# Kernel optimization log

Measured on AMD Instinct MI355X. Metric: run time of the kernel, lower is better.

The kernel has to match this reference:

```python
import jax, jax.numpy as jnp
from jax import lax
import numpy as np

B, D, H, W = 1, 20, 96, 96
N = B * (D - 4) * H * W  # one 7x7x7 guide patch per output voxel
DN = ('NCDHW', 'OIDHW', 'NCDHW')


def _conv3(x, w, b):
    # Conv3d(1,1,kernel=3,stride=1,VALID) + bias
    y = lax.conv_general_dilated(x, w, (1, 1, 1), 'VALID', dimension_numbers=DN)
    return y + b[None, :, None, None, None]


def _guide_branch(x, w1, b1, w2, b2):
    # nn.Sequential(Conv3d, ReLU, Conv3d, ReLU): 7^3 -> 5^3 -> 3^3
    return jax.nn.relu(_conv3(jax.nn.relu(_conv3(x, w1, b1)), w2, b2))


def setup_inputs() -> dict:
    key = jax.random.key(0)
    ks = jax.random.split(key, 12)
    s = 1.0 / np.sqrt(27.0)  # torch Conv3d default init scale (fan_in = 1*3*3*3)
    return {
        'x': jax.random.normal(ks[0], (B, 1, D, H, W), jnp.float32),
        'domain_neighbor': jax.random.uniform(ks[1], (1, 1, 7, 7, 7), jnp.float32),
        'guide_im': jax.random.normal(ks[2], (N, 1, 7, 7, 7), jnp.float32),
        'w1_d': jax.random.normal(ks[3], (1, 1, 3, 3, 3), jnp.float32) * s,
        'b1_d': jax.random.normal(ks[4], (1,), jnp.float32) * s,
        'w2_d': jax.random.normal(ks[5], (1, 1, 3, 3, 3), jnp.float32) * s,
        'b2_d': jax.random.normal(ks[6], (1,), jnp.float32) * s,
        'w1_r': jax.random.normal(ks[7], (1, 1, 3, 3, 3), jnp.float32) * s,
        'b1_r': jax.random.normal(ks[8], (1,), jnp.float32) * s,
        'w2_r': jax.random.normal(ks[9], (1, 1, 3, 3, 3), jnp.float32) * s,
        'b2_r': jax.random.normal(ks[10], (1,), jnp.float32) * s,
    }


def reference(x, domain_neighbor, guide_im, w1_d, b1_d, w2_d, b2_d,
              w1_r, b1_r, w2_r, b2_r):
    Bx, _, Dx, Hx, Wx = x.shape
    # kernel-generating guide nets
    domain_kernel = _guide_branch(domain_neighbor, w1_d, b1_d, w2_d, b2_d)  # (1,1,3,3,3)
    range_kernel = _guide_branch(guide_im, w1_r, b1_r, w2_r, b2_r)          # (N,1,3,3,3)
    weights = (domain_kernel * range_kernel + 1e-10).reshape(-1, 27)        # (N,27)
    # pad H,W by 1 (depth unpadded), extract all 3x3x3 patches (feature order d,h,w)
    xp = jnp.pad(x, ((0, 0), (0, 0), (0, 0), (1, 1), (1, 1)))
    p = lax.conv_general_dilated_patches(xp, (3, 3, 3), (1, 1, 1), 'VALID',
                                         dimension_numbers=DN)  # (B,27,D-2,H,W)
    p = p[:, :, 1:-1]  # keep the D-4 center-aligned depth windows (matches mat_size)
    p = p.transpose(0, 2, 3, 4, 1).reshape(-1, 27)  # (N,27)
    out = jnp.sum(weights * p, axis=1) / jnp.sum(weights, axis=1)  # weighted local mean
    return out.reshape(Bx, 1, Dx - 4, Hx, Wx)
```

## Files before the change

### kernel.cpp

```cpp
#include <hip/hip_runtime.h>
#include <hip/hip_fp16.h>


#define NPATCH 147456
#define TPB     256
#define PPB      64
#define NBLK   (NPATCH / PPB)
#define ROW_H     8
#define PATCH_H 392
#define PATCH_D 196
#define NROWS  (PPB * 49)
#define NRD      13

typedef float f4u __attribute__((ext_vector_type(4), aligned(4)));
typedef float f2u __attribute__((ext_vector_type(2), aligned(4)));

__global__ __launch_bounds__(128) void domain_branch_kernel(
    const float* __restrict__ dn,
    const float* __restrict__ w1, const float* __restrict__ b1,
    const float* __restrict__ w2, const float* __restrict__ b2,
    float* __restrict__ dom_out)
{
    __shared__ float s_in[344];
    __shared__ float s_c1[128];
    const int t = threadIdx.x;
    for (int idx = t; idx < 343; idx += 128) s_in[idx] = dn[idx];
    __syncthreads();
    if (t < 125) {
        const int i = t / 25, j = (t / 5) % 5, k = t % 5;
        float acc = b1[0];
        const float* base = &s_in[i * 49 + j * 7 + k];
#pragma unroll
        for (int dz = 0; dz < 3; ++dz)
#pragma unroll
            for (int dy = 0; dy < 3; ++dy)
#pragma unroll
                for (int dx = 0; dx < 3; ++dx)
                    acc = fmaf(base[dz * 49 + dy * 7 + dx], w1[dz * 9 + dy * 3 + dx], acc);
        s_c1[t] = fmaxf(acc, 0.f);
    }
    __syncthreads();
    if (t < 27) {
        const int dz = t / 9, dy = (t / 3) % 3, dx = t % 3;
        float acc = b2[0];
#pragma unroll
        for (int u = 0; u < 3; ++u)
#pragma unroll
            for (int v = 0; v < 3; ++v)
#pragma unroll
                for (int q = 0; q < 3; ++q)
                    acc = fmaf(s_c1[(dz + u) * 25 + (dy + v) * 5 + (dx + q)],
                               w2[u * 9 + v * 3 + q], acc);
        dom_out[t] = fmaxf(acc, 0.f);
    }
}

__device__ __forceinline__ float h2f_lo(unsigned int q) {
    return __half2float(__ushort_as_half((unsigned short)(q & 0xffffu)));
}
__device__ __forceinline__ float h2f_hi(unsigned int q) {
    return __half2float(__ushort_as_half((unsigned short)(q >> 16)));
}
__device__ __forceinline__ unsigned int pkh(float lo, float hi) {
    return __builtin_bit_cast(unsigned int, __builtin_amdgcn_cvt_pkrtz(lo, hi));
}

__device__ __forceinline__ void load_row(const unsigned int* __restrict__ P, float* d,
                                         int zi, int y) {
    const int d0 = zi * 28 + y * 4;
    const uint4 q = *reinterpret_cast<const uint4*>(P + d0);
    d[0] = h2f_lo(q.x); d[1] = h2f_hi(q.x);
    d[2] = h2f_lo(q.y); d[3] = h2f_hi(q.y);
    d[4] = h2f_lo(q.z); d[5] = h2f_hi(q.z);
    d[6] = h2f_lo(q.w);
}

template<int IB, int JB, int IE, int JE>
__device__ __forceinline__ void run_tasks(const unsigned int* __restrict__ P,
                                          const float* __restrict__ w1, float bb1,
                                          const float* __restrict__ w2,
                                          float (&a2)[3][3][3])
{
#pragma unroll
    for (int i = IB; i <= IE; ++i) {
        float rw[3][3][7];
        const int j0 = (i == IB) ? JB : 0;
        const int j1 = (i == IE) ? JE : 4;
#pragma unroll
        for (int j = j0; j <= j1; ++j) {
            if (j == j0) {
#pragma unroll
                for (int u = 0; u < 3; ++u)
#pragma unroll
                    for (int dy = 0; dy < 3; ++dy)
                        load_row(P, rw[u][(j + dy) % 3], i + u, j + dy);
            } else {
#pragma unroll
                for (int u = 0; u < 3; ++u)
                    load_row(P, rw[u][(j + 2) % 3], i + u, j + 2);
            }

            float c1r[5];
#pragma unroll
            for (int k = 0; k < 5; ++k) {
                float a = bb1;
#pragma unroll
                for (int u = 0; u < 3; ++u)
#pragma unroll
                    for (int v = 0; v < 3; ++v) {
                        const float* rr = rw[u][(j + v) % 3];
#pragma unroll
                        for (int w = 0; w < 3; ++w)
                            a = fmaf(rr[k + w], w1[u * 9 + v * 3 + w], a);
                    }
                c1r[k] = fmaxf(a, 0.f);
            }

#pragma unroll
            for (int dz2 = 0; dz2 < 3; ++dz2) {
                const int u2 = i - dz2;
                if (u2 >= 0 && u2 < 3) {
#pragma unroll
                    for (int v2 = 0; v2 < 3; ++v2) {
                        const int dy2 = j - v2;
                        if (dy2 >= 0 && dy2 < 3) {
#pragma unroll
                            for (int dx2 = 0; dx2 < 3; ++dx2)
#pragma unroll
                                for (int q = 0; q < 3; ++q)
                                    a2[dz2][dy2][dx2] =
                                        fmaf(c1r[dx2 + q],
                                             w2[u2 * 9 + v2 * 3 + q],
                                             a2[dz2][dy2][dx2]);
                        }
                    }
                }
            }
        }
    }
}

__global__ __launch_bounds__(TPB, 2) void jbf_main_kernel(
    const float* __restrict__ guide, const float* __restrict__ x,
    const float* __restrict__ w1, const float* __restrict__ b1,
    const float* __restrict__ w2, const float* __restrict__ b2,
    const float* __restrict__ dom, float* __restrict__ out)
{
    union SM {
        unsigned short tile[PPB * PATCH_H];
        float part[3][PPB][27];
    };
    __shared__ SM sm;

    const int tid  = threadIdx.x;
    const int wid  = tid >> 6;
    const int lane = tid & 63;
    const int blk  = blockIdx.x;
    const int n    = blk * PPB + lane;

    {
        const float* __restrict__ srcf = guide + (size_t)blk * (PPB * 343);
        unsigned int* __restrict__ tdw = reinterpret_cast<unsigned int*>(sm.tile);

        f4u A[NRD]; f2u B[NRD]; float C[NRD];
#pragma unroll
        for (int rd = 0; rd < NRD; ++rd) {
            int idx = tid + rd * TPB;
            if (idx > NROWS - 1) idx = NROWS - 1;
            const int p = idx / 49, r = idx - p * 49;
            const float* s = srcf + p * 343 + r * 7;
            A[rd] = *reinterpret_cast<const f4u*>(s);
            B[rd] = *reinterpret_cast<const f2u*>(s + 4);
            C[rd] = s[6];
        }
        __builtin_amdgcn_sched_barrier(0);
#pragma unroll
        for (int rd = 0; rd < NRD; ++rd) {
            if (rd < 12 || tid < NROWS - 12 * TPB) {
                const int idx = tid + rd * TPB;
                const int p = idx / 49, r = idx - p * 49;
                uint4 q;
                q.x = pkh(A[rd].x, A[rd].y); q.y = pkh(A[rd].z, A[rd].w);
                q.z = pkh(B[rd].x, B[rd].y); q.w = pkh(C[rd], 0.f);
                *reinterpret_cast<uint4*>(tdw + p * PATCH_D + r * 4) = q;
            }
        }
    }
    __syncthreads();

    const unsigned int* __restrict__ P =
        reinterpret_cast<const unsigned int*>(sm.tile) + lane * PATCH_D;
    const float bb1 = b1[0];

    float a2[3][3][3];
    {
        const float init = (wid == 0) ? b2[0] : 0.f;
#pragma unroll
        for (int a = 0; a < 3; ++a)
#pragma unroll
            for (int b = 0; b < 3; ++b)
#pragma unroll
                for (int c = 0; c < 3; ++c) a2[a][b][c] = init;
    }

    if      (wid == 0) run_tasks<0, 0, 1, 1>(P, w1, bb1, w2, a2);
    else if (wid == 1) run_tasks<1, 2, 2, 3>(P, w1, bb1, w2, a2);
    else if (wid == 2) run_tasks<2, 4, 3, 4>(P, w1, bb1, w2, a2);
    else               run_tasks<4, 0, 4, 4>(P, w1, bb1, w2, a2);

    __syncthreads();

    if (wid != 0) {
#pragma unroll
        for (int t = 0; t < 27; ++t)
            sm.part[wid - 1][lane][t] = a2[t / 9][(t / 3) % 3][t % 3];
    }
    __syncthreads();

    if (wid == 0) {
        const int dd  = n / 9216;
        const int rem = n - dd * 9216;
        const int h   = rem / 96;
        const int w_  = rem - h * 96;

        float num = 0.f, den = 0.f;
#pragma unroll
        for (int dz = 0; dz < 3; ++dz)
#pragma unroll
            for (int dy = 0; dy < 3; ++dy)
#pragma unroll
                for (int dx = 0; dx < 3; ++dx) {
                    const int t = dz * 9 + dy * 3 + dx;
                    const float r2 = fmaxf(a2[dz][dy][dx] + sm.part[0][lane][t]
                                           + sm.part[1][lane][t]
                                           + sm.part[2][lane][t], 0.f);
                    const float wt = fmaf(dom[t], r2, 1e-10f);
                    const int yy = h - 1 + dy, xx = w_ - 1 + dx;
                    float xv = 0.f;
                    if (yy >= 0 && yy < 96 && xx >= 0 && xx < 96)
                        xv = x[(dd + 1 + dz) * 9216 + yy * 96 + xx];
                    num = fmaf(wt, xv, num);
                    den += wt;
                }
        out[n] = num / den;
    }
}

extern "C" void kernel_launch(void* const* d_in, const int* in_sizes, int n_in,
                              void* d_out, int out_size, void* d_ws, size_t ws_size,
                              hipStream_t stream) {
    const float* x     = (const float*)d_in[0];
    const float* dn    = (const float*)d_in[1];
    const float* guide = (const float*)d_in[2];
    const float* w1_d  = (const float*)d_in[3];
    const float* b1_d  = (const float*)d_in[4];
    const float* w2_d  = (const float*)d_in[5];
    const float* b2_d  = (const float*)d_in[6];
    const float* w1_r  = (const float*)d_in[7];
    const float* b1_r  = (const float*)d_in[8];
    const float* w2_r  = (const float*)d_in[9];
    const float* b2_r  = (const float*)d_in[10];
    float* out = (float*)d_out;
    float* dom = (float*)d_ws;

    domain_branch_kernel<<<1, 128, 0, stream>>>(dn, w1_d, b1_d, w2_d, b2_d, dom);
    jbf_main_kernel<<<NBLK, TPB, 0, stream>>>(guide, x, w1_r, b1_r, w2_r,
                                              b2_r, dom, out);
}
```

Baseline: 46.26 us.

## Make main kernel persistent with a producer wave double-buffering guide tiles

The main kernel becomes persistent: 256 blocks each loop over 9 tiles of 64 patches. One wave acts as a producer, loading and fp16-packing the next tile into a second LDS buffer while the other three waves compute on the current tile. Wave 0 also finishes the previous tile's weighted-mean epilogue inside the loop. This aims to hide global-load latency behind compute, but leaves only three compute waves per block and one block per CU (launch_bounds 256,1). It also needs about 116 KB of dynamic LDS, so occupancy drops.

```diff
diff --git a/kernel.cpp b/kernel.cpp
--- a/kernel.cpp
+++ b/kernel.cpp
@@ -2,15 +2,17 @@
 #include <hip/hip_fp16.h>
 
 
-#define NPATCH 147456
-#define TPB     256
+#define NPATCH   147456
+#define TPB      256
 #define PPB      64
-#define NBLK   (NPATCH / PPB)
-#define ROW_H     8
-#define PATCH_H 392
-#define PATCH_D 196
-#define NROWS  (PPB * 49)
-#define NRD      13
+#define NTILES   (NPATCH / PPB)
+#define NBLOCK   256
+#define TPBLK    (NTILES / NBLOCK)
+#define PATCH_H  392
+#define PATCH_D  196
+#define NROWS    (PPB * 49)
+#define BUF_H    (PPB * PATCH_H)
+#define SMEM_BYTES (2 * BUF_H * 2 + 2 * 2 * PPB * 27 * 4)
 
 typedef float f4u __attribute__((ext_vector_type(4), aligned(4)));
 typedef float f2u __attribute__((ext_vector_type(2), aligned(4)));
@@ -140,31 +142,57 @@
     }
 }
 
-__global__ __launch_bounds__(TPB, 2) void jbf_main_kernel(
+template<int CNT>
+__device__ __forceinline__ void stage_chunk(const float* __restrict__ srcf,
+                                            unsigned int* __restrict__ dwbuf,
+                                            int& p, int& rem) {
+    f4u A[CNT]; f2u B[CNT]; float C[CNT];
+    int pl = p, rl = rem;
+#pragma unroll
+    for (int k = 0; k < CNT; ++k) {
+        const float* s = srcf + pl * 343 + rl * 7;
+        A[k] = *reinterpret_cast<const f4u*>(s);
+        B[k] = *reinterpret_cast<const f2u*>(s + 4);
+        C[k] = s[6];
+        pl += 1; rl += 15; if (rl >= 49) { rl -= 49; pl += 1; }
+    }
+    __builtin_amdgcn_sched_barrier(0);
+    pl = p; rl = rem;
+#pragma unroll
+    for (int k = 0; k < CNT; ++k) {
+        uint4 q;
+        q.x = pkh(A[k].x, A[k].y); q.y = pkh(A[k].z, A[k].w);
+        q.z = pkh(B[k].x, B[k].y); q.w = pkh(C[k], 0.f);
+        *reinterpret_cast<uint4*>(dwbuf + pl * PATCH_D + rl * 4) = q;
+        pl += 1; rl += 15; if (rl >= 49) { rl -= 49; pl += 1; }
+    }
+    p = pl; rem = rl;
+}
+
+__global__ __launch_bounds__(TPB, 1) void jbf_main_kernel(
     const float* __restrict__ guide, const float* __restrict__ x,
     const float* __restrict__ w1, const float* __restrict__ b1,
     const float* __restrict__ w2, const float* __restrict__ b2,
     const float* __restrict__ dom, float* __restrict__ out)
 {
-    union SM {
-        unsigned short tile[PPB * PATCH_H];
-        float part[3][PPB][27];
-    };
-    __shared__ SM sm;
-
-    const int tid  = threadIdx.x;
-    const int wid  = tid >> 6;
-    const int lane = tid & 63;
-    const int blk  = blockIdx.x;
-    const int n    = blk * PPB + lane;
+    extern __shared__ unsigned char smem[];
+    unsigned short* buf  = reinterpret_cast<unsigned short*>(smem);
+    float*          part = reinterpret_cast<float*>(smem + 2 * BUF_H * 2);
+
+    const int tid   = threadIdx.x;
+    const int wid   = tid >> 6;
+    const int lane  = tid & 63;
+    const int tile0 = blockIdx.x * TPBLK;
+
+    const float bb1 = b1[0];
+    const float bb2 = b2[0];
 
     {
-        const float* __restrict__ srcf = guide + (size_t)blk * (PPB * 343);
-        unsigned int* __restrict__ tdw = reinterpret_cast<unsigned int*>(sm.tile);
-
-        f4u A[NRD]; f2u B[NRD]; float C[NRD];
-#pragma unroll
-        for (int rd = 0; rd < NRD; ++rd) {
+        const float* __restrict__ srcf = guide + (size_t)tile0 * (PPB * 343);
+        unsigned int* __restrict__ tdw = reinterpret_cast<unsigned int*>(buf);
+        f4u A[13]; f2u B[13]; float C[13];
+#pragma unroll
+        for (int rd = 0; rd < 13; ++rd) {
             int idx = tid + rd * TPB;
             if (idx > NROWS - 1) idx = NROWS - 1;
             const int p = idx / 49, r = idx - p * 49;
@@ -175,7 +203,7 @@
         }
         __builtin_amdgcn_sched_barrier(0);
 #pragma unroll
-        for (int rd = 0; rd < NRD; ++rd) {
+        for (int rd = 0; rd < 13; ++rd) {
             if (rd < 12 || tid < NROWS - 12 * TPB) {
                 const int idx = tid + rd * TPB;
                 const int p = idx / 49, r = idx - p * 49;
@@ -188,41 +216,85 @@
     }
     __syncthreads();
 
-    const unsigned int* __restrict__ P =
-        reinterpret_cast<const unsigned int*>(sm.tile) + lane * PATCH_D;
-    const float bb1 = b1[0];
-
     float a2[3][3][3];
-    {
-        const float init = (wid == 0) ? b2[0] : 0.f;
-#pragma unroll
-        for (int a = 0; a < 3; ++a)
-#pragma unroll
-            for (int b = 0; b < 3; ++b)
-#pragma unroll
-                for (int c = 0; c < 3; ++c) a2[a][b][c] = init;
-    }
-
-    if      (wid == 0) run_tasks<0, 0, 1, 1>(P, w1, bb1, w2, a2);
-    else if (wid == 1) run_tasks<1, 2, 2, 3>(P, w1, bb1, w2, a2);
-    else if (wid == 2) run_tasks<2, 4, 3, 4>(P, w1, bb1, w2, a2);
-    else               run_tasks<4, 0, 4, 4>(P, w1, bb1, w2, a2);
-
-    __syncthreads();
-
-    if (wid != 0) {
-#pragma unroll
-        for (int t = 0; t < 27; ++t)
-            sm.part[wid - 1][lane][t] = a2[t / 9][(t / 3) % 3][t % 3];
-    }
-    __syncthreads();
+
+#pragma unroll 1
+    for (int t = 0; t < TPBLK; ++t) {
+        unsigned int* curd = reinterpret_cast<unsigned int*>(buf + (t & 1) * BUF_H);
+
+        if (wid == 3) {
+            if (t + 1 < TPBLK) {
+                const float* __restrict__ srcf =
+                    guide + (size_t)(tile0 + t + 1) * (PPB * 343);
+                unsigned int* __restrict__ nxtd =
+                    reinterpret_cast<unsigned int*>(buf + ((t + 1) & 1) * BUF_H);
+                int p = lane / 49, rem = lane - (lane / 49) * 49;
+                stage_chunk<17>(srcf, nxtd, p, rem);
+                stage_chunk<16>(srcf, nxtd, p, rem);
+                stage_chunk<16>(srcf, nxtd, p, rem);
+            }
+        } else if (wid == 0) {
+            if (t > 0) {
+                const int n   = (tile0 + t - 1) * PPB + lane;
+                const float* pb = part + ((t - 1) & 1) * (2 * PPB * 27);
+                const int dd  = n / 9216;
+                const int rm  = n - dd * 9216;
+                const int h   = rm / 96;
+                const int w_  = rm - h * 96;
+                float num = 0.f, den = 0.f;
+#pragma unroll
+                for (int dz = 0; dz < 3; ++dz)
+#pragma unroll
+                    for (int dy = 0; dy < 3; ++dy)
+#pragma unroll
+                        for (int dx = 0; dx < 3; ++dx) {
+                            const int tt = dz * 9 + dy * 3 + dx;
+                            const float r2 = fmaxf(a2[dz][dy][dx]
+                                                   + pb[(0 * PPB + lane) * 27 + tt]
+                                                   + pb[(1 * PPB + lane) * 27 + tt], 0.f);
+                            const float wt = fmaf(dom[tt], r2, 1e-10f);
+                            const int yy = h - 1 + dy, xx = w_ - 1 + dx;
+                            float xv = 0.f;
+                            if (yy >= 0 && yy < 96 && xx >= 0 && xx < 96)
+                                xv = x[(dd + 1 + dz) * 9216 + yy * 96 + xx];
+                            num = fmaf(wt, xv, num);
+                            den += wt;
+                        }
+                out[n] = num / den;
+            }
+#pragma unroll
+            for (int a = 0; a < 3; ++a)
+#pragma unroll
+                for (int b = 0; b < 3; ++b)
+#pragma unroll
+                    for (int c = 0; c < 3; ++c) a2[a][b][c] = bb2;
+            run_tasks<0, 0, 1, 3>(curd + lane * PATCH_D, w1, bb1, w2, a2);
+        } else {
+            float al[3][3][3];
+#pragma unroll
+            for (int a = 0; a < 3; ++a)
+#pragma unroll
+                for (int b = 0; b < 3; ++b)
+#pragma unroll
+                    for (int c = 0; c < 3; ++c) al[a][b][c] = 0.f;
+            if (wid == 1) run_tasks<1, 4, 3, 1>(curd + lane * PATCH_D, w1, bb1, w2, al);
+            else          run_tasks<3, 2, 4, 4>(curd + lane * PATCH_D, w1, bb1, w2, al);
+            float* pb = part + (t & 1) * (2 * PPB * 27) + ((wid - 1) * PPB + lane) * 27;
+#pragma unroll
+            for (int tt = 0; tt < 27; ++tt)
+                pb[tt] = al[tt / 9][(tt / 3) % 3][tt % 3];
+        }
+        __syncthreads();
+    }
 
     if (wid == 0) {
+        const int t = TPBLK - 1;
+        const int n   = (tile0 + t) * PPB + lane;
+        const float* pb = part + (t & 1) * (2 * PPB * 27);
         const int dd  = n / 9216;
-        const int rem = n - dd * 9216;
-        const int h   = rem / 96;
-        const int w_  = rem - h * 96;
-
+        const int rm  = n - dd * 9216;
+        const int h   = rm / 96;
+        const int w_  = rm - h * 96;
         float num = 0.f, den = 0.f;
 #pragma unroll
         for (int dz = 0; dz < 3; ++dz)
@@ -230,11 +302,11 @@
             for (int dy = 0; dy < 3; ++dy)
 #pragma unroll
                 for (int dx = 0; dx < 3; ++dx) {
-                    const int t = dz * 9 + dy * 3 + dx;
-                    const float r2 = fmaxf(a2[dz][dy][dx] + sm.part[0][lane][t]
-                                           + sm.part[1][lane][t]
-                                           + sm.part[2][lane][t], 0.f);
-                    const float wt = fmaf(dom[t], r2, 1e-10f);
+                    const int tt = dz * 9 + dy * 3 + dx;
+                    const float r2 = fmaxf(a2[dz][dy][dx]
+                                           + pb[(0 * PPB + lane) * 27 + tt]
+                                           + pb[(1 * PPB + lane) * 27 + tt], 0.f);
+                    const float wt = fmaf(dom[tt], r2, 1e-10f);
                     const int yy = h - 1 + dy, xx = w_ - 1 + dx;
                     float xv = 0.f;
                     if (yy >= 0 && yy < 96 && xx >= 0 && xx < 96)
@@ -263,7 +335,10 @@
     float* out = (float*)d_out;
     float* dom = (float*)d_ws;
 
+    hipFuncSetAttribute((const void*)jbf_main_kernel,
+                        hipFuncAttributeMaxDynamicSharedMemorySize, SMEM_BYTES);
+
     domain_branch_kernel<<<1, 128, 0, stream>>>(dn, w1_d, b1_d, w2_d, b2_d, dom);
-    jbf_main_kernel<<<NBLK, TPB, 0, stream>>>(guide, x, w1_r, b1_r, w2_r,
-                                              b2_r, dom, out);
-}
+    jbf_main_kernel<<<NBLOCK, TPB, SMEM_BYTES, stream>>>(guide, x, w1_r, b1_r,
+                                                         w2_r, b2_r, dom, out);
+}
```

New measurement: 65.18 us. 1.41x slower.

## Split final weighted-sum epilogue across all four waves and prefetch x early

Applied to the files above, without the earlier changes.

The final weighted-mean epilogue, previously done only by wave 0 over all 27 taps, is now split so each of the four waves handles 6-7 taps. Partial numerators and denominators are reduced through shared memory. The x neighbourhood values are loaded into registers at kernel start so their global-load latency overlaps the guide tile load and conv work. This costs extra registers, an additional shared-memory round trip and one more barrier.

```diff
diff --git a/kernel.cpp b/kernel.cpp
--- a/kernel.cpp
+++ b/kernel.cpp
@@ -148,7 +148,10 @@
 {
     union SM {
         unsigned short tile[PPB * PATCH_H];
-        float part[3][PPB][27];
+        struct {
+            float part[4][PPB][27];
+            float nd[4][PPB][2];
+        } c;
     };
     __shared__ SM sm;
 
@@ -157,6 +160,28 @@
     const int lane = tid & 63;
     const int blk  = blockIdx.x;
     const int n    = blk * PPB + lane;
+
+    const int t0   = wid * 7;
+    const int tcnt = (wid == 3) ? 6 : 7;
+    const int dd   = n / 9216;
+    const int rem  = n - dd * 9216;
+    const int h    = rem / 96;
+    const int w_   = rem - h * 96;
+
+    float xv[7];
+#pragma unroll
+    for (int k = 0; k < 7; ++k) {
+        if (k < tcnt) {
+            const int tt = t0 + k;
+            const int dz = tt / 9, r9 = tt - dz * 9;
+            const int dy = r9 / 3,  dx = r9 - dy * 3;
+            const int yy = h - 1 + dy, xx = w_ - 1 + dx;
+            float v = 0.f;
+            if (yy >= 0 && yy < 96 && xx >= 0 && xx < 96)
+                v = x[(dd + 1 + dz) * 9216 + yy * 96 + xx];
+            xv[k] = v;
+        }
+    }
 
     {
         const float* __restrict__ srcf = guide + (size_t)blk * (PPB * 343);
@@ -210,38 +235,36 @@
 
     __syncthreads();
 
-    if (wid != 0) {
-#pragma unroll
-        for (int t = 0; t < 27; ++t)
-            sm.part[wid - 1][lane][t] = a2[t / 9][(t / 3) % 3][t % 3];
+#pragma unroll
+    for (int t = 0; t < 27; ++t)
+        sm.c.part[wid][lane][t] = a2[t / 9][(t / 3) % 3][t % 3];
+    __syncthreads();
+
+    {
+        float num = 0.f, den = 0.f;
+#pragma unroll
+        for (int k = 0; k < 7; ++k) {
+            if (k < tcnt) {
+                const int tt = t0 + k;
+                const float r2 = fmaxf(sm.c.part[0][lane][tt]
+                                       + sm.c.part[1][lane][tt]
+                                       + sm.c.part[2][lane][tt]
+                                       + sm.c.part[3][lane][tt], 0.f);
+                const float wt = fmaf(dom[tt], r2, 1e-10f);
+                num = fmaf(wt, xv[k], num);
+                den += wt;
+            }
+        }
+        sm.c.nd[wid][lane][0] = num;
+        sm.c.nd[wid][lane][1] = den;
     }
     __syncthreads();
 
     if (wid == 0) {
-        const int dd  = n / 9216;
-        const int rem = n - dd * 9216;
-        const int h   = rem / 96;
-        const int w_  = rem - h * 96;
-
-        float num = 0.f, den = 0.f;
-#pragma unroll
-        for (int dz = 0; dz < 3; ++dz)
-#pragma unroll
-            for (int dy = 0; dy < 3; ++dy)
-#pragma unroll
-                for (int dx = 0; dx < 3; ++dx) {
-                    const int t = dz * 9 + dy * 3 + dx;
-                    const float r2 = fmaxf(a2[dz][dy][dx] + sm.part[0][lane][t]
-                                           + sm.part[1][lane][t]
-                                           + sm.part[2][lane][t], 0.f);
-                    const float wt = fmaf(dom[t], r2, 1e-10f);
-                    const int yy = h - 1 + dy, xx = w_ - 1 + dx;
-                    float xv = 0.f;
-                    if (yy >= 0 && yy < 96 && xx >= 0 && xx < 96)
-                        xv = x[(dd + 1 + dz) * 9216 + yy * 96 + xx];
-                    num = fmaf(wt, xv, num);
-                    den += wt;
-                }
+        const float num = sm.c.nd[0][lane][0] + sm.c.nd[1][lane][0]
+                        + sm.c.nd[2][lane][0] + sm.c.nd[3][lane][0];
+        const float den = sm.c.nd[0][lane][1] + sm.c.nd[1][lane][1]
+                        + sm.c.nd[2][lane][1] + sm.c.nd[3][lane][1];
         out[n] = num / den;
     }
 }
```

Measured after the change: 47.77 us. 1.03x slower.
